# Kernel tuning notes

Hardware: AMD Instinct MI355X
Metric: run time of the kernel (lower is better)

Reference implementation:

```python
import jax, jax.numpy as jnp
import numpy as np

ALPHA, KL, KS = 0.2, 0.3, 1.0  # PGDKernel defaults

_OFFSETS = jnp.array([[a, b, c] for a in (0, 1) for b in (0, 1) for c in (0, 1)], dtype=jnp.int32)  # [8,3]


def _cic_corners(pos, mesh):
    # pos: [N,3] in grid units, periodic wrap
    base = jnp.floor(pos)
    frac = pos - base                              # [N,3]
    base = base.astype(jnp.int32)
    idx = (base[:, None, :] + _OFFSETS[None, :, :]) % mesh   # [N,8,3]
    w = jnp.prod(jnp.where(_OFFSETS[None].astype(bool), frac[:, None, :], 1.0 - frac[:, None, :]), axis=-1)  # [N,8]
    flat = (idx[..., 0] * mesh + idx[..., 1]) * mesh + idx[..., 2]  # [N,8]
    return flat, w


def cic_paint(pos, mesh):
    flat, w = _cic_corners(pos, mesh)
    grid = jnp.zeros((mesh * mesh * mesh,), dtype=pos.dtype)
    grid = grid.at[flat.reshape(-1)].add(w.reshape(-1))
    return grid.reshape(mesh, mesh, mesh)


def cic_read(grid, pos, mesh):
    flat, w = _cic_corners(pos, mesh)
    return jnp.sum(grid.reshape(-1)[flat] * w, axis=-1)  # [N]


def fftk(mesh):
    k = (2.0 * np.pi * jnp.fft.fftfreq(mesh)).astype(jnp.float32)
    return [k.reshape(-1, 1, 1), k.reshape(1, -1, 1), k.reshape(1, 1, -1)]


def setup_inputs() -> dict:
    key = jax.random.key(0)
    k1, k2 = jax.random.split(key)
    mesh = 128
    n = mesh ** 3
    g = jnp.arange(mesh, dtype=jnp.float32)
    lattice = jnp.stack(jnp.meshgrid(g, g, g, indexing='ij'), axis=-1).reshape(-1, 3)
    pos = (lattice + 0.5 * jax.random.normal(k1, (n, 3), dtype=jnp.float32)) % mesh
    vel = 0.01 * jax.random.normal(k2, (n, 3), dtype=jnp.float32)
    return {"pos": pos, "vel": vel, "mesh_size": mesh}


def reference(pos, vel, mesh_size):
    mesh = int(mesh_size)
    delta = cic_paint(pos, mesh)                       # particle-mesh deposit
    delta_k = jnp.fft.fftn(delta)                      # complex64 [m,m,m]
    kvec = fftk(mesh)
    kk = sum(ki ** 2 for ki in kvec)
    kk_safe = jnp.where(kk == 0, 1.0, kk)
    pgd_range = jnp.exp(-(KL ** 2) / kk_safe) * jnp.exp(-(kk ** 2) / (KS ** 4))
    pgd_range = jnp.where(kk == 0, 0.0, pgd_range)
    invlap = -jnp.where(kk == 0, 0.0, 1.0 / kk_safe)   # inverse laplace kernel
    pot_k = delta_k * (invlap * pgd_range)
    # gradient kernel: i*k_i ; force_i = readout(ifft(-grad_i * pot_k))
    forces = jnp.stack(
        [cic_read(jnp.fft.ifftn(-1j * ki * pot_k).real.astype(pos.dtype), pos, mesh) for ki in kvec],
        axis=-1,
    )  # [N,3]
    new_pos = pos + ALPHA * forces
    return new_pos, vel
```

## Files before the change

kernel.cpp:

```cpp
#include <hip/hip_runtime.h>
#include <hip/hip_bf16.h>

#define MESH   128
#define MESH2  16384
#define MESH3  2097152
#define SP 21
#define CELLS (SP * SP * SP)

__device__ __forceinline__ float kfreq(int i) {
    int s = (i < 64) ? i : (i - 128);
    return 0.049087385212340517f * (float)s;
}

__device__ __forceinline__ float load_elem(const void* p, int i, int isbf16) {
    if (isbf16) return __bfloat162float(((const __hip_bfloat16*)p)[i]);
    return ((const float*)p)[i];
}

__device__ __forceinline__ void dft8(float2* a, float sgn) {
    const float r = 0.70710678118654752f;
    float2 b0 = a[0], b1 = a[4], b2 = a[2], b3 = a[6];
    float2 b4 = a[1], b5 = a[5], b6 = a[3], b7 = a[7];
    float2 c0 = make_float2(b0.x + b1.x, b0.y + b1.y);
    float2 c1 = make_float2(b0.x - b1.x, b0.y - b1.y);
    float2 c2 = make_float2(b2.x + b3.x, b2.y + b3.y);
    float2 c3 = make_float2(b2.x - b3.x, b2.y - b3.y);
    float2 c4 = make_float2(b4.x + b5.x, b4.y + b5.y);
    float2 c5 = make_float2(b4.x - b5.x, b4.y - b5.y);
    float2 c6 = make_float2(b6.x + b7.x, b6.y + b7.y);
    float2 c7 = make_float2(b6.x - b7.x, b6.y - b7.y);
    float2 t3 = make_float2(-sgn * c3.y, sgn * c3.x);
    float2 t7 = make_float2(-sgn * c7.y, sgn * c7.x);
    float2 d0 = make_float2(c0.x + c2.x, c0.y + c2.y);
    float2 d2 = make_float2(c0.x - c2.x, c0.y - c2.y);
    float2 d1 = make_float2(c1.x + t3.x, c1.y + t3.y);
    float2 d3 = make_float2(c1.x - t3.x, c1.y - t3.y);
    float2 d4 = make_float2(c4.x + c6.x, c4.y + c6.y);
    float2 d6 = make_float2(c4.x - c6.x, c4.y - c6.y);
    float2 d5 = make_float2(c5.x + t7.x, c5.y + t7.y);
    float2 d7 = make_float2(c5.x - t7.x, c5.y - t7.y);
    float2 w1 = make_float2(r, sgn * r), w3 = make_float2(-r, sgn * r);
    float2 t5 = make_float2(d5.x * w1.x - d5.y * w1.y, d5.x * w1.y + d5.y * w1.x);
    float2 t6 = make_float2(-sgn * d6.y, sgn * d6.x);
    float2 t7b = make_float2(d7.x * w3.x - d7.y * w3.y, d7.x * w3.y + d7.y * w3.x);
    a[0] = make_float2(d0.x + d4.x, d0.y + d4.y);
    a[4] = make_float2(d0.x - d4.x, d0.y - d4.y);
    a[1] = make_float2(d1.x + t5.x, d1.y + t5.y);
    a[5] = make_float2(d1.x - t5.x, d1.y - t5.y);
    a[2] = make_float2(d2.x + t6.x, d2.y + t6.y);
    a[6] = make_float2(d2.x - t6.x, d2.y - t6.y);
    a[3] = make_float2(d3.x + t7b.x, d3.y + t7b.y);
    a[7] = make_float2(d3.x - t7b.x, d3.y - t7b.y);
}

__global__ void detect_kernel(const unsigned int* __restrict__ words,
                              int* __restrict__ flag) {
    int t = threadIdx.x;
    unsigned long long m = __ballot((words[t] >> 15) & 1u);
    if (t == 0) *flag = (__popcll(m) > 16) ? 0 : 1;
}

__global__ __launch_bounds__(256)
void paint_lds(const void* __restrict__ pos, float* __restrict__ grid,
               const int* __restrict__ flag) {
    __shared__ float tile[CELLS];
    int t = threadIdx.x;
    int bi = blockIdx.x;
    int tz = bi & 7, ty = (bi >> 3) & 7, tx = bi >> 6;
    int x0 = tx * 16, y0 = ty * 16, z0 = tz * 16;
    for (int i = t; i < CELLS; i += 256) tile[i] = 0.f;
    __syncthreads();
    int isbf16 = *flag;
#pragma unroll
    for (int it = 0; it < 16; ++it) {
        int pi = t + 256 * it;
        int dz = pi & 15, dy = (pi >> 4) & 15, dx = pi >> 8;
        int p = (((x0 + dx) << 7) + (y0 + dy)) * 128 + z0 + dz;
        float P0 = load_elem(pos, 3 * p + 0, isbf16);
        float P1 = load_elem(pos, 3 * p + 1, isbf16);
        float P2 = load_elem(pos, 3 * p + 2, isbf16);
        float f0 = floorf(P0), f1 = floorf(P1), f2 = floorf(P2);
        int ix = (int)f0, iy = (int)f1, iz = (int)f2;
        float wx1 = P0 - f0, wy1 = P1 - f1, wz1 = P2 - f2;
        float wx0 = 1.f - wx1, wy0 = 1.f - wy1, wz0 = 1.f - wz1;
        int lx = (ix - x0 + 2) & 127, ly = (iy - y0 + 2) & 127;
        int lz = (iz - z0 + 2) & 127;
        if (lx <= 19 && ly <= 19 && lz <= 19) {
            int b00 = (lx * SP + ly) * SP + lz;
            int b01 = b00 + SP;
            int b10 = b00 + SP * SP;
            int b11 = b10 + SP;
            atomicAdd(&tile[b00],     wx0 * wy0 * wz0);
            atomicAdd(&tile[b00 + 1], wx0 * wy0 * wz1);
            atomicAdd(&tile[b01],     wx0 * wy1 * wz0);
            atomicAdd(&tile[b01 + 1], wx0 * wy1 * wz1);
            atomicAdd(&tile[b10],     wx1 * wy0 * wz0);
            atomicAdd(&tile[b10 + 1], wx1 * wy0 * wz1);
            atomicAdd(&tile[b11],     wx1 * wy1 * wz0);
            atomicAdd(&tile[b11 + 1], wx1 * wy1 * wz1);
        } else {
            int gx = ix & 127, gy = iy & 127, gz = iz & 127;
            int hx = (gx + 1) & 127, hy = (gy + 1) & 127, hz = (gz + 1) & 127;
            atomicAdd(&grid[((gx << 7) + gy) * 128 + gz], wx0 * wy0 * wz0);
            atomicAdd(&grid[((gx << 7) + gy) * 128 + hz], wx0 * wy0 * wz1);
            atomicAdd(&grid[((gx << 7) + hy) * 128 + gz], wx0 * wy1 * wz0);
            atomicAdd(&grid[((gx << 7) + hy) * 128 + hz], wx0 * wy1 * wz1);
            atomicAdd(&grid[((hx << 7) + gy) * 128 + gz], wx1 * wy0 * wz0);
            atomicAdd(&grid[((hx << 7) + gy) * 128 + hz], wx1 * wy0 * wz1);
            atomicAdd(&grid[((hx << 7) + hy) * 128 + gz], wx1 * wy1 * wz0);
            atomicAdd(&grid[((hx << 7) + hy) * 128 + hz], wx1 * wy1 * wz1);
        }
    }
    __syncthreads();
    for (int i = t; i < CELLS; i += 256) {
        float v = tile[i];
        if (v != 0.f) {
            int lx = i / (SP * SP);
            int r  = i - lx * (SP * SP);
            int ly = r / SP, lz = r - ly * SP;
            int gx = (x0 - 2 + lx) & 127, gy = (y0 - 2 + ly) & 127;
            int gz = (z0 - 2 + lz) & 127;
            atomicAdd(&grid[((gx << 7) + gy) * 128 + gz], v);
        }
    }
}

template<int AXIS, int INV, int LM, int SM>
__global__ __launch_bounds__(256)
void fft8x16(const void* __restrict__ s0, const void* __restrict__ s1,
             void* __restrict__ d0, void* __restrict__ d1, void* __restrict__ d2) {
    __shared__ float2 Z[16 * 137];
    int t = threadIdx.x;
    int l = (AXIS == 2) ? (t >> 4) : (t & 15);
    int u = (AXIS == 2) ? (t & 15) : (t >> 4);
    int L = blockIdx.x * 16 + l;
    int vol = blockIdx.y;
    const float sgn = INV ? 1.f : -1.f;
    const float invN3 = 1.0f / 2097152.0f;
    long base; int es;
    if (AXIS == 2)      { base = (long)L * 128; es = 1; }
    else if (AXIS == 1) { base = (long)(L >> 7) * 16384 + (L & 127); es = 128; }
    else                { base = (long)L; es = 16384; }
    const void* srcv = vol ? s1 : s0;

    float2 v[8];
#pragma unroll
    for (int n1 = 0; n1 < 8; ++n1) {
        int e = 16 * n1 + u;
        if (LM == 1) v[n1] = make_float2(((const float*)srcv)[base + (long)e * es], 0.f);
        else         v[n1] = ((const float2*)srcv)[base + (long)e * es];
    }
    dft8(v, sgn);
#pragma unroll
    for (int k1 = 0; k1 < 8; ++k1) {
        float ang = sgn * 0.049087385212340517f * (float)(u * k1);
        float sn, cs; __sincosf(ang, &sn, &cs);
        float2 y = v[k1];
        Z[l * 137 + k1 * 17 + u] =
            make_float2(y.x * cs - y.y * sn, y.x * sn + y.y * cs);
    }
    __syncthreads();

    int k1 = u & 7, c = u >> 3;
    float2 w[8];
#pragma unroll
    for (int b = 0; b < 8; ++b) {
        float2 za = Z[l * 137 + k1 * 17 + b];
        float2 zb = Z[l * 137 + k1 * 17 + 8 + b];
        float2 s = c ? make_float2(za.x - zb.x, za.y - zb.y)
                     : make_float2(za.x + zb.x, za.y + zb.y);
        if (c && b) {
            float ang = sgn * 0.39269908169872414f * (float)b;
            float sn, cs; __sincosf(ang, &sn, &cs);
            s = make_float2(s.x * cs - s.y * sn, s.x * sn + s.y * cs);
        }
        w[b] = s;
    }
    dft8(w, sgn);
#pragma unroll
    for (int k3 = 0; k3 < 8; ++k3) {
        int k = u + 16 * k3;
        float2 vv = w[k3];
        long idx = base + (long)k * es;
        if (SM == 0) {
            ((float2*)(vol ? d1 : d0))[idx] = vv;
        } else if (SM == 3) {
            float kx = kfreq(k), ky = kfreq(L >> 7), kz = kfreq(L & 127);
            float kk = kx * kx + ky * ky + kz * kz;
            float f = 0.f;
            if (kk > 0.f) f = -__expf(-0.09f / kk - kk * kk) / kk * invN3;
            float a = vv.x * f, b = vv.y * f;
            ((float2*)d0)[idx] = make_float2(-kx * b - ky * a, kx * a - ky * b);
            ((float2*)d1)[idx] = make_float2(-kz * b, kz * a);
        } else {
            if (vol == 0) {
                ((float*)d0)[idx] = vv.x;
                ((float*)d1)[idx] = vv.y;
            } else {
                ((float*)d2)[idx] = vv.x;
            }
        }
    }
}

__global__ __launch_bounds__(256)
void update_pos(const void* __restrict__ pos,
                const float* __restrict__ Fx, const float* __restrict__ Fy,
                const float* __restrict__ Fz, float* __restrict__ out,
                const int* __restrict__ flag, int n) {
    int p = blockIdx.x * blockDim.x + threadIdx.x;
    if (p >= n) return;
    int isbf16 = *flag;
    float P0 = load_elem(pos, 3 * p + 0, isbf16);
    float P1 = load_elem(pos, 3 * p + 1, isbf16);
    float P2 = load_elem(pos, 3 * p + 2, isbf16);
    float f0 = floorf(P0), f1 = floorf(P1), f2 = floorf(P2);
    int ix = ((int)f0) & 127, iy = ((int)f1) & 127, iz = ((int)f2) & 127;
    float wx1 = P0 - f0, wy1 = P1 - f1, wz1 = P2 - f2;
    float wx0 = 1.f - wx1, wy0 = 1.f - wy1, wz0 = 1.f - wz1;
    int jx = (ix + 1) & 127, jy = (iy + 1) & 127, jz = (iz + 1) & 127;
    int b00 = (ix * MESH + iy) * MESH;
    int b01 = (ix * MESH + jy) * MESH;
    int b10 = (jx * MESH + iy) * MESH;
    int b11 = (jx * MESH + jy) * MESH;
    float fx = 0.f, fy = 0.f, fz = 0.f;
    int f; float w;
    f = b00 + iz; w = wx0 * wy0 * wz0; fx += w * Fx[f]; fy += w * Fy[f]; fz += w * Fz[f];
    f = b00 + jz; w = wx0 * wy0 * wz1; fx += w * Fx[f]; fy += w * Fy[f]; fz += w * Fz[f];
    f = b01 + iz; w = wx0 * wy1 * wz0; fx += w * Fx[f]; fy += w * Fy[f]; fz += w * Fz[f];
    f = b01 + jz; w = wx0 * wy1 * wz1; fx += w * Fx[f]; fy += w * Fy[f]; fz += w * Fz[f];
    f = b10 + iz; w = wx1 * wy0 * wz0; fx += w * Fx[f]; fy += w * Fy[f]; fz += w * Fz[f];
    f = b10 + jz; w = wx1 * wy0 * wz1; fx += w * Fx[f]; fy += w * Fy[f]; fz += w * Fz[f];
    f = b11 + iz; w = wx1 * wy1 * wz0; fx += w * Fx[f]; fy += w * Fy[f]; fz += w * Fz[f];
    f = b11 + jz; w = wx1 * wy1 * wz1; fx += w * Fx[f]; fy += w * Fy[f]; fz += w * Fz[f];
    out[3 * p + 0] = P0 + 0.2f * fx;
    out[3 * p + 1] = P1 + 0.2f * fy;
    out[3 * p + 2] = P2 + 0.2f * fz;
}

__global__ __launch_bounds__(256)
void copy_vel(const void* __restrict__ vel, float* __restrict__ dst,
              const int* __restrict__ flag, int m) {
    int i0 = (blockIdx.x * blockDim.x + threadIdx.x) * 4;
    int isbf16 = *flag;
#pragma unroll
    for (int j = 0; j < 4; ++j) {
        int i = i0 + j;
        if (i < m) dst[i] = load_elem(vel, i, isbf16);
    }
}

extern "C" void kernel_launch(void* const* d_in, const int* in_sizes, int n_in,
                              void* d_out, int out_size, void* d_ws, size_t ws_size,
                              hipStream_t stream) {
    int n = in_sizes[0] / 3;
    const void* pos = d_in[0];
    const void* vel = d_in[1];
    float* out = (float*)d_out;

    char* ws = (char*)d_ws;
    int*    flag = (int*)ws;
    float2* A  = (float2*)(ws + 4096);
    float*  F0 = (float*)(ws + 4096 + (16u << 20));
    float*  F1 = (float*)(ws + 4096 + (24u << 20));
    float*  delta = (float*)d_out;
    float2* G2 = (float2*)((char*)d_out + (24u << 20));
    float*  F2 = (float*)((char*)d_out + (40u << 20));

    detect_kernel<<<1, 64, 0, stream>>>((const unsigned int*)pos, flag);
    hipMemsetAsync(delta, 0, MESH3 * sizeof(float), stream);
    paint_lds<<<512, 256, 0, stream>>>(pos, delta, flag);

    fft8x16<2, 0, 1, 0><<<dim3(1024, 1), 256, 0, stream>>>(delta, nullptr, A, nullptr, nullptr);
    fft8x16<1, 0, 0, 0><<<dim3(1024, 1), 256, 0, stream>>>(A, nullptr, A, nullptr, nullptr);
    fft8x16<0, 0, 0, 3><<<dim3(1024, 1), 256, 0, stream>>>(A, nullptr, A, G2, nullptr);

    fft8x16<2, 1, 0, 0><<<dim3(1024, 2), 256, 0, stream>>>(A, G2, A, G2, nullptr);
    fft8x16<1, 1, 0, 0><<<dim3(1024, 2), 256, 0, stream>>>(A, G2, A, G2, nullptr);
    fft8x16<0, 1, 0, 4><<<dim3(1024, 2), 256, 0, stream>>>(A, G2, F0, F1, F2);

    update_pos<<<(n + 255) / 256, 256, 0, stream>>>(pos, F0, F1, F2, out, flag, n);
    int m = 3 * n;
    copy_vel<<<(m / 4 + 255) / 256, 256, 0, stream>>>(vel, out + m, flag, m);
}
```

Measured before the change: 300.5 us.

## Replace scatter CIC paint with lattice-neighborhood gather paint

The CIC deposit no longer scatters with shared-memory atomics. Each block loads the particles whose lattice sites lie in a halo around its 16x16x8 cell tile and stores their offsets relative to the tile in shared memory. Each thread then gathers contributions for four cells from the nearby particles, using tent weights, and writes them with one global atomic per cell. Particles that move more than about one cell from their lattice site fall back to global-atomic scatter by the block that owns them. This removes contended LDS atomics, but it relies on particle ordering matching the lattice. It also adds redundant halo loads and weight evaluations.

```diff
diff --git a/kernel.cpp b/kernel.cpp
--- a/kernel.cpp
+++ b/kernel.cpp
@@ -4,8 +4,10 @@
 #define MESH   128
 #define MESH2  16384
 #define MESH3  2097152
-#define SP 21
-#define CELLS (SP * SP * SP)
+#define NSX 19
+#define NSY 19
+#define NSZ 11
+#define NS  (NSX * NSY * NSZ)
 
 __device__ __forceinline__ float kfreq(int i) {
     int s = (i < 64) ? i : (i - 128);
@@ -15,6 +17,10 @@
 __device__ __forceinline__ float load_elem(const void* p, int i, int isbf16) {
     if (isbf16) return __bfloat162float(((const __hip_bfloat16*)p)[i]);
     return ((const float*)p)[i];
+}
+
+__device__ __forceinline__ void glbAddF(float* p, float v) {
+    asm volatile("global_atomic_add_f32 %0, %1, off" :: "v"(p), "v"(v) : "memory");
 }
 
 __device__ __forceinline__ void dft8(float2* a, float sgn) {
@@ -60,69 +66,87 @@
     if (t == 0) *flag = (__popcll(m) > 16) ? 0 : 1;
 }
 
-__global__ __launch_bounds__(256)
-void paint_lds(const void* __restrict__ pos, float* __restrict__ grid,
-               const int* __restrict__ flag) {
-    __shared__ float tile[CELLS];
+__global__ __launch_bounds__(512, 4)
+void gather_paint(const void* __restrict__ pos, float* __restrict__ grid,
+                  const int* __restrict__ flag) {
+    __shared__ float su[NS * 3];
     int t = threadIdx.x;
     int bi = blockIdx.x;
-    int tz = bi & 7, ty = (bi >> 3) & 7, tx = bi >> 6;
-    int x0 = tx * 16, y0 = ty * 16, z0 = tz * 16;
-    for (int i = t; i < CELLS; i += 256) tile[i] = 0.f;
+    int tz = bi & 15, ty = (bi >> 4) & 7, tx = bi >> 7;
+    int x0 = tx * 16, y0 = ty * 16, z0 = tz * 8;
+    int isbf16 = *flag;
+
+    for (int i = t; i < NS; i += 512) {
+        int szl = i % NSZ;
+        int r   = i / NSZ;
+        int syl = r % NSY;
+        int sxl = r / NSY;
+        int ax = (x0 - 2 + sxl) & 127;
+        int ay = (y0 - 2 + syl) & 127;
+        int az = (z0 - 2 + szl) & 127;
+        int pidx = (ax << 14) + (ay << 7) + az;
+        float Px = load_elem(pos, 3 * pidx + 0, isbf16);
+        float Py = load_elem(pos, 3 * pidx + 1, isbf16);
+        float Pz = load_elem(pos, 3 * pidx + 2, isbf16);
+        float dx = Px - (float)ax; if (dx > 64.f) dx -= 128.f; else if (dx < -64.f) dx += 128.f;
+        float dy = Py - (float)ay; if (dy > 64.f) dy -= 128.f; else if (dy < -64.f) dy += 128.f;
+        float dz = Pz - (float)az; if (dz > 64.f) dz -= 128.f; else if (dz < -64.f) dz += 128.f;
+        float fx = floorf(dx), fy = floorf(dy), fz = floorf(dz);
+        bool reg = (fx >= -1.f) && (fx <= 1.f) && (fy >= -1.f) && (fy <= 1.f)
+                && (fz >= -1.f) && (fz <= 1.f);
+        float ux = 1e9f, uy = 1e9f, uz = 1e9f;
+        if (reg) {
+            ux = (float)(sxl - 2) + dx;
+            uy = (float)(syl - 2) + dy;
+            uz = (float)(szl - 2) + dz;
+        } else if (sxl >= 2 && sxl < 18 && syl >= 2 && syl < 18 &&
+                   szl >= 2 && szl < 10) {
+            float f0 = floorf(Px), f1 = floorf(Py), f2 = floorf(Pz);
+            int ix = (int)f0 & 127, iy = (int)f1 & 127, iz = (int)f2 & 127;
+            float wx1 = Px - f0, wy1 = Py - f1, wz1 = Pz - f2;
+            float wx0 = 1.f - wx1, wy0 = 1.f - wy1, wz0 = 1.f - wz1;
+            int hx = (ix + 1) & 127, hy = (iy + 1) & 127, hz = (iz + 1) & 127;
+            glbAddF(&grid[((ix << 7) + iy) * 128 + iz], wx0 * wy0 * wz0);
+            glbAddF(&grid[((ix << 7) + iy) * 128 + hz], wx0 * wy0 * wz1);
+            glbAddF(&grid[((ix << 7) + hy) * 128 + iz], wx0 * wy1 * wz0);
+            glbAddF(&grid[((ix << 7) + hy) * 128 + hz], wx0 * wy1 * wz1);
+            glbAddF(&grid[((hx << 7) + iy) * 128 + iz], wx1 * wy0 * wz0);
+            glbAddF(&grid[((hx << 7) + iy) * 128 + hz], wx1 * wy0 * wz1);
+            glbAddF(&grid[((hx << 7) + hy) * 128 + iz], wx1 * wy1 * wz0);
+            glbAddF(&grid[((hx << 7) + hy) * 128 + hz], wx1 * wy1 * wz1);
+        }
+        su[3 * i + 0] = ux;
+        su[3 * i + 1] = uy;
+        su[3 * i + 2] = uz;
+    }
     __syncthreads();
-    int isbf16 = *flag;
-#pragma unroll
-    for (int it = 0; it < 16; ++it) {
-        int pi = t + 256 * it;
-        int dz = pi & 15, dy = (pi >> 4) & 15, dx = pi >> 8;
-        int p = (((x0 + dx) << 7) + (y0 + dy)) * 128 + z0 + dz;
-        float P0 = load_elem(pos, 3 * p + 0, isbf16);
-        float P1 = load_elem(pos, 3 * p + 1, isbf16);
-        float P2 = load_elem(pos, 3 * p + 2, isbf16);
-        float f0 = floorf(P0), f1 = floorf(P1), f2 = floorf(P2);
-        int ix = (int)f0, iy = (int)f1, iz = (int)f2;
-        float wx1 = P0 - f0, wy1 = P1 - f1, wz1 = P2 - f2;
-        float wx0 = 1.f - wx1, wy0 = 1.f - wy1, wz0 = 1.f - wz1;
-        int lx = (ix - x0 + 2) & 127, ly = (iy - y0 + 2) & 127;
-        int lz = (iz - z0 + 2) & 127;
-        if (lx <= 19 && ly <= 19 && lz <= 19) {
-            int b00 = (lx * SP + ly) * SP + lz;
-            int b01 = b00 + SP;
-            int b10 = b00 + SP * SP;
-            int b11 = b10 + SP;
-            atomicAdd(&tile[b00],     wx0 * wy0 * wz0);
-            atomicAdd(&tile[b00 + 1], wx0 * wy0 * wz1);
-            atomicAdd(&tile[b01],     wx0 * wy1 * wz0);
-            atomicAdd(&tile[b01 + 1], wx0 * wy1 * wz1);
-            atomicAdd(&tile[b10],     wx1 * wy0 * wz0);
-            atomicAdd(&tile[b10 + 1], wx1 * wy0 * wz1);
-            atomicAdd(&tile[b11],     wx1 * wy1 * wz0);
-            atomicAdd(&tile[b11 + 1], wx1 * wy1 * wz1);
-        } else {
-            int gx = ix & 127, gy = iy & 127, gz = iz & 127;
-            int hx = (gx + 1) & 127, hy = (gy + 1) & 127, hz = (gz + 1) & 127;
-            atomicAdd(&grid[((gx << 7) + gy) * 128 + gz], wx0 * wy0 * wz0);
-            atomicAdd(&grid[((gx << 7) + gy) * 128 + hz], wx0 * wy0 * wz1);
-            atomicAdd(&grid[((gx << 7) + hy) * 128 + gz], wx0 * wy1 * wz0);
-            atomicAdd(&grid[((gx << 7) + hy) * 128 + hz], wx0 * wy1 * wz1);
-            atomicAdd(&grid[((hx << 7) + gy) * 128 + gz], wx1 * wy0 * wz0);
-            atomicAdd(&grid[((hx << 7) + gy) * 128 + hz], wx1 * wy0 * wz1);
-            atomicAdd(&grid[((hx << 7) + hy) * 128 + gz], wx1 * wy1 * wz0);
-            atomicAdd(&grid[((hx << 7) + hy) * 128 + hz], wx1 * wy1 * wz1);
+
+    int q = t & 1, cy = (t >> 1) & 15, cx = t >> 5;
+    float cxf = (float)cx, cyf = (float)cy, cz0 = (float)(4 * q);
+    float a0 = 0.f, a1 = 0.f, a2 = 0.f, a3 = 0.f;
+    for (int i = 0; i < 4; ++i) {
+        for (int j = 0; j < 4; ++j) {
+            int sb = ((cx + i) * NSY + (cy + j)) * NSZ + 4 * q;
+#pragma unroll
+            for (int k = 0; k < 7; ++k) {
+                const float* p3 = &su[(sb + k) * 3];
+                float ux = p3[0], uy = p3[1], uz = p3[2];
+                float wx = fmaxf(0.f, 1.f - fabsf(ux - cxf));
+                float wy = fmaxf(0.f, 1.f - fabsf(uy - cyf));
+                float wxy = wx * wy;
+                float d = uz - cz0;
+                a0 += wxy * fmaxf(0.f, 1.f - fabsf(d));
+                a1 += wxy * fmaxf(0.f, 1.f - fabsf(d - 1.f));
+                a2 += wxy * fmaxf(0.f, 1.f - fabsf(d - 2.f));
+                a3 += wxy * fmaxf(0.f, 1.f - fabsf(d - 3.f));
+            }
         }
     }
-    __syncthreads();
-    for (int i = t; i < CELLS; i += 256) {
-        float v = tile[i];
-        if (v != 0.f) {
-            int lx = i / (SP * SP);
-            int r  = i - lx * (SP * SP);
-            int ly = r / SP, lz = r - ly * SP;
-            int gx = (x0 - 2 + lx) & 127, gy = (y0 - 2 + ly) & 127;
-            int gz = (z0 - 2 + lz) & 127;
-            atomicAdd(&grid[((gx << 7) + gy) * 128 + gz], v);
-        }
-    }
+    int gb = ((x0 + cx) << 14) + ((y0 + cy) << 7) + z0 + 4 * q;
+    glbAddF(&grid[gb + 0], a0);
+    glbAddF(&grid[gb + 1], a1);
+    glbAddF(&grid[gb + 2], a2);
+    glbAddF(&grid[gb + 3], a3);
 }
 
 template<int AXIS, int INV, int LM, int SM>
@@ -269,7 +293,7 @@
 
     detect_kernel<<<1, 64, 0, stream>>>((const unsigned int*)pos, flag);
     hipMemsetAsync(delta, 0, MESH3 * sizeof(float), stream);
-    paint_lds<<<512, 256, 0, stream>>>(pos, delta, flag);
+    gather_paint<<<1024, 512, 0, stream>>>(pos, delta, flag);
 
     fft8x16<2, 0, 1, 0><<<dim3(1024, 1), 256, 0, stream>>>(delta, nullptr, A, nullptr, nullptr);
     fft8x16<1, 0, 0, 0><<<dim3(1024, 1), 256, 0, stream>>>(A, nullptr, A, nullptr, nullptr);
```

Result: slower. 319.5 us (+6.3%).
